# Kernel optimization log

Measured on AMD Instinct MI355X. Metric: run time of the kernel, lower is better.

## Reference

```python
import jax, jax.numpy as jnp
import numpy as np

EMBED = 256
HEADS = 8
LEVELS = 4
POINTS = 4
HD = EMBED // HEADS  # 32


def _bilinear_sample(v, grid):
    """torch.F.grid_sample(mode='bilinear', padding_mode='zeros', align_corners=False).
    v: (B, C, H, W); grid: (B, Q, P, 2) with xy coords in [-1, 1].
    Returns (B, C, Q, P).
    """
    B, C, H, W = v.shape
    x = (grid[..., 0] + 1.0) * (W * 0.5) - 0.5
    y = (grid[..., 1] + 1.0) * (H * 0.5) - 0.5
    x0f = jnp.floor(x)
    y0f = jnp.floor(y)
    wx = x - x0f
    wy = y - y0f
    x0 = x0f.astype(jnp.int32)
    y0 = y0f.astype(jnp.int32)
    vf = v.reshape(B, C, H * W)

    def corner(xi, yi, w):
        valid = (xi >= 0) & (xi < W) & (yi >= 0) & (yi < H)
        idx = jnp.clip(yi, 0, H - 1) * W + jnp.clip(xi, 0, W - 1)  # (B, Q, P)
        g = jax.vmap(lambda vb, ib: jnp.take(vb, ib, axis=1))(vf, idx.reshape(B, -1))
        g = g.reshape(B, C, idx.shape[1], idx.shape[2])  # (B, C, Q, P)
        return g * (w * valid.astype(v.dtype))[:, None]

    return (corner(x0, y0, (1 - wx) * (1 - wy))
            + corner(x0 + 1, y0, wx * (1 - wy))
            + corner(x0, y0 + 1, (1 - wx) * wy)
            + corner(x0 + 1, y0 + 1, wx * wy))


def setup_inputs() -> dict:
    key = jax.random.key(0)
    ks = jax.random.split(key, 16)
    N, Q, D = 2, 8192, EMBED
    inp = {
        'query': jax.random.normal(ks[0], (N, Q, D), jnp.float32),
        'feat0': jax.random.normal(ks[1], (N, D, 64, 64), jnp.float32),
        'feat1': jax.random.normal(ks[2], (N, D, 32, 32), jnp.float32),
        'feat2': jax.random.normal(ks[3], (N, D, 16, 16), jnp.float32),
        'feat3': jax.random.normal(ks[4], (N, D, 8, 8), jnp.float32),
        'reference_points': jax.random.uniform(ks[5], (N, Q, 2), jnp.float32),
        # params stored as (in, out); equivalent math to torch Linear's x @ W.T + b
        'W_off': jax.random.normal(ks[6], (D, HEADS * LEVELS * POINTS * 2), jnp.float32) * 0.01,
        'b_off': jax.random.normal(ks[7], (HEADS * LEVELS * POINTS * 2,), jnp.float32) * 0.01,
        'W_attn': jax.random.normal(ks[8], (D, HEADS * LEVELS * POINTS), jnp.float32) * 0.02,
        'b_attn': jax.random.normal(ks[9], (HEADS * LEVELS * POINTS,), jnp.float32) * 0.02,
        'W_val': jax.random.normal(ks[10], (D, D), jnp.float32) * (1.0 / np.sqrt(D)),
        'b_val': jnp.zeros((D,), jnp.float32),
        'W_out': jax.random.normal(ks[11], (D, D), jnp.float32) * (1.0 / np.sqrt(D)),
        'b_out': jnp.zeros((D,), jnp.float32),
    }
    return inp


def reference(query, feat0, feat1, feat2, feat3, reference_points,
              W_off, b_off, W_attn, b_attn, W_val, b_val, W_out, b_out):
    feats = [feat0, feat1, feat2, feat3]
    N, Q, D = query.shape
    # offset / attention-weight projections
    off = (query @ W_off + b_off).reshape(N, Q, HEADS, LEVELS, POINTS, 2)
    attn = (query @ W_attn + b_attn).reshape(N, Q, HEADS, LEVELS, POINTS)
    # reference points (N,Q,2) -> (N,Q,L,2)
    ref = jnp.broadcast_to(reference_points[:, :, None, :], (N, Q, LEVELS, 2))
    # value projection (1x1 conv) per level, split heads -> (N*H, hd, H_l, W_l)
    vals = [(jnp.einsum('bchw,cd->bdhw', f, W_val) + b_val[None, :, None, None])
            .reshape(N * HEADS, HD, f.shape[2], f.shape[3]) for f in feats]
    # flatten batch*heads
    off = off.transpose(0, 2, 1, 3, 4, 5).reshape(N * HEADS, Q, LEVELS, POINTS, 2)
    attn = attn.transpose(0, 2, 1, 3, 4).reshape(N * HEADS, Q, LEVELS, POINTS)
    refh = jnp.broadcast_to(ref[:, None], (N, HEADS, Q, LEVELS, 2)).reshape(N * HEADS, Q, LEVELS, 2)
    loc = refh[:, :, :, None, :] + off                 # (NH, Q, L, P, 2) in [0,1]
    grid = 2.0 * loc - 1.0                             # [-1, 1]
    # per-level bilinear sampling -> (NH, hd, Q, L, P)
    sampled = jnp.stack([_bilinear_sample(vals[l], grid[:, :, l]) for l in range(LEVELS)], axis=-2)
    # softmax over levels*points
    aw = jax.nn.softmax(attn.reshape(N * HEADS, Q, LEVELS * POINTS), axis=-1)
    aw = jnp.nan_to_num(aw).reshape(N * HEADS, Q, LEVELS, POINTS)
    out = jnp.einsum('bcqlp,bqlp->bcq', sampled, aw)   # (NH, hd, Q)
    out = out.reshape(N, HEADS, HD, Q).transpose(0, 3, 1, 2).reshape(N, Q, D)
    return out @ W_out + b_out
```

## Files before the change

kernel.cpp:

```cpp
#include <hip/hip_runtime.h>
#include <math.h>

#define NB 2
#define QN 8192
#define DIM 256
#define S_TOT 5440

typedef unsigned int uint32;
typedef _Float16 f16;
typedef __attribute__((ext_vector_type(8))) _Float16 h8;
typedef __attribute__((ext_vector_type(2))) _Float16 h2;
typedef __attribute__((ext_vector_type(4))) float f32x4;
typedef __attribute__((ext_vector_type(4))) uint32 u32x4;

__global__ __launch_bounds__(256) void prep_w_kernel(
    const float* __restrict__ W_off, const float* __restrict__ W_attn,
    const float* __restrict__ W_val, const float* __restrict__ W_out,
    f16* __restrict__ Wcat_t, f16* __restrict__ Wval_t, f16* __restrict__ Wout_t) {
  const int t = blockIdx.x;
  const float* src; f16* dst; int S, tb;
  if (t < 8)       { src = W_off;  dst = Wcat_t;             S = 256; tb = t; }
  else if (t < 12) { src = W_attn; dst = Wcat_t + 256 * 256; S = 128; tb = t - 8; }
  else if (t < 20) { src = W_val;  dst = Wval_t;             S = 256; tb = t - 12; }
  else             { src = W_out;  dst = Wout_t;             S = 256; tb = t - 20; }
  const int s0 = tb * 32, c0 = blockIdx.y * 32;

  __shared__ float tile[32][33];
  const int tx = threadIdx.x & 31, ty = threadIdx.x >> 5;
#pragma unroll
  for (int j = 0; j < 4; ++j) {
    const int c = c0 + ty + j * 8;
    tile[ty + j * 8][tx] = src[(size_t)c * S + s0 + tx];
  }
  __syncthreads();
#pragma unroll
  for (int j = 0; j < 4; ++j) {
    const int srow = s0 + ty + j * 8;
    dst[(size_t)srow * 256 + c0 + tx] = (f16)tile[tx][ty + j * 8];
  }
}

__global__ __launch_bounds__(256) void gemm_fused_kernel(
    const float* __restrict__ f0, const float* __restrict__ f1,
    const float* __restrict__ f2, const float* __restrict__ f3,
    const float* __restrict__ query,
    const f16* __restrict__ Wval_t, const f16* __restrict__ Wcat_t,
    const float* __restrict__ b_val, const float* __restrict__ b_off,
    const float* __restrict__ b_attn,
    f16* __restrict__ vals, f16* __restrict__ offb, f16* __restrict__ attnb) {
  __shared__ f16 As[64][256];
  __shared__ f16 Bs[64][256];
  const int t = blockIdx.x;
  const int tid = threadIdx.x;
  const bool isval = (t < 170);
  const size_t r0 = (size_t)(isval ? t : t - 170) * 64;
  const int NC = isval ? 4 : 6;
  const f16* Bt = isval ? Wval_t : Wcat_t;

  const int row = tid >> 5, slot = tid & 31;
  const int lane = tid & 63;

  if (isval) {
    const int b = (t >= 85) ? 1 : 0;
    const int tl = t - 85 * b;
    const float* fsrc; int HW, sl0;
    if (tl < 64)      { fsrc = f0; HW = 4096; sl0 = tl * 64; }
    else if (tl < 80) { fsrc = f1; HW = 1024; sl0 = (tl - 64) * 64; }
    else if (tl < 84) { fsrc = f2; HW = 256;  sl0 = (tl - 80) * 64; }
    else              { fsrc = f3; HW = 64;   sl0 = 0; }
    fsrc += (size_t)b * 256 * HW + sl0;
    const int cw = (tid >> 6) * 64 + (lane >> 4);
    const int s4 = (lane & 15) * 4;
#pragma unroll
    for (int pass = 0; pass < 16; ++pass) {
      const int c = cw + pass * 4;
      const float4 v = *(const float4*)(fsrc + (size_t)c * HW + s4);
      const int sl = c >> 3;
#pragma unroll
      for (int j = 0; j < 4; ++j) {
        const int r = s4 + j;
        const int ph = (sl & 24) | ((sl ^ r) & 7);
        As[r][ph * 8 + (c & 7)] = (f16)((const float*)&v)[j];
      }
    }
  } else {
#pragma unroll
    for (int i = 0; i < 8; ++i) {
      const int r = i * 8 + row;
      const int ph = (slot & 24) | ((slot ^ r) & 7);
      const float* ga = query + (r0 + r) * 256 + slot * 8;
      const float4 u0 = *(const float4*)ga;
      const float4 u1 = *(const float4*)(ga + 4);
      h8 hv = {(f16)u0.x, (f16)u0.y, (f16)u0.z, (f16)u0.w,
               (f16)u1.x, (f16)u1.y, (f16)u1.z, (f16)u1.w};
      *(h8*)&As[r][ph * 8] = hv;
    }
  }

  const int wid = tid >> 6;
  const int wr = (wid >> 1) * 32, wc = (wid & 1) * 32;
  const int l15 = lane & 15, l4 = lane >> 4;

  u32x4 bpre[8];
#pragma unroll
  for (int i = 0; i < 8; ++i) {
    bpre[i] = *(const u32x4*)(Bt + (size_t)(i * 8 + row) * 256 + slot * 8);
  }

  h8 areg[8][2];

  for (int c = 0; c < NC; ++c) {
    __syncthreads();
#pragma unroll
    for (int i = 0; i < 8; ++i) {
      const int r = i * 8 + row;
      const int ph = (slot & 24) | ((slot ^ r) & 7);
      *(u32x4*)&Bs[r][ph * 8] = bpre[i];
    }
    __syncthreads();

    if (c + 1 < NC) {
#pragma unroll
      for (int i = 0; i < 8; ++i) {
        bpre[i] = *(const u32x4*)(Bt + (size_t)((c + 1) * 64 + i * 8 + row) * 256 + slot * 8);
      }
    }

    f32x4 acc[2][2] = {};
#pragma unroll
    for (int ks = 0; ks < 8; ++ks) {
      const int slot2 = ks * 4 + l4;
      if (c == 0) {
#pragma unroll
        for (int m = 0; m < 2; ++m) {
          const int r = wr + m * 16 + l15;
          const int ph = (slot2 & 24) | ((slot2 ^ r) & 7);
          areg[ks][m] = *(const h8*)&As[r][ph * 8];
        }
      }
      h8 b[2];
#pragma unroll
      for (int n = 0; n < 2; ++n) {
        const int r = wc + n * 16 + l15;
        const int ph = (slot2 & 24) | ((slot2 ^ r) & 7);
        b[n] = *(const h8*)&Bs[r][ph * 8];
      }
#pragma unroll
      for (int m = 0; m < 2; ++m)
#pragma unroll
        for (int n = 0; n < 2; ++n)
          acc[m][n] = __builtin_amdgcn_mfma_f32_16x16x32_f16(areg[ks][m], b[n], acc[m][n], 0, 0, 0);
    }

#pragma unroll
    for (int m = 0; m < 2; ++m)
#pragma unroll
      for (int n = 0; n < 2; ++n)
#pragma unroll
        for (int r = 0; r < 4; ++r) {
          const size_t rw = r0 + wr + m * 16 + l4 * 4 + r;
          const int col = c * 64 + wc + n * 16 + l15;
          const float v = acc[m][n][r];
          if (isval) {
            vals[rw * 256 + col] = (f16)(v + b_val[col]);
          } else if (col < 256) {
            offb[rw * 256 + col] = (f16)(v + b_off[col]);
          } else {
            attnb[rw * 128 + (col - 256)] = (f16)(v + b_attn[col - 256]);
          }
        }
  }
}

__global__ __launch_bounds__(256) void gemm_out_kernel(
    const f16* __restrict__ A, const f16* __restrict__ Bt,
    const float* __restrict__ bias, float* __restrict__ out) {
  __shared__ f16 As[64][256];
  __shared__ f16 Bs[64][256];
  const int tid = threadIdx.x;
  const size_t r0 = (size_t)blockIdx.x * 64;

  const int row = tid >> 5, slot = tid & 31;
#pragma unroll
  for (int i = 0; i < 8; ++i) {
    const int r = i * 8 + row;
    const int ph = (slot & 24) | ((slot ^ r) & 7);
    *(u32x4*)&As[r][ph * 8] = *(const u32x4*)(A + (r0 + r) * 256 + slot * 8);
  }

  const int wid = tid >> 6, lane = tid & 63;
  const int wr = (wid >> 1) * 32, wc = (wid & 1) * 32;
  const int l15 = lane & 15, l4 = lane >> 4;

  u32x4 bpre[8];
#pragma unroll
  for (int i = 0; i < 8; ++i) {
    bpre[i] = *(const u32x4*)(Bt + (size_t)(i * 8 + row) * 256 + slot * 8);
  }

  h8 areg[8][2];

  for (int c = 0; c < 4; ++c) {
    __syncthreads();
#pragma unroll
    for (int i = 0; i < 8; ++i) {
      const int r = i * 8 + row;
      const int ph = (slot & 24) | ((slot ^ r) & 7);
      *(u32x4*)&Bs[r][ph * 8] = bpre[i];
    }
    __syncthreads();

    if (c + 1 < 4) {
#pragma unroll
      for (int i = 0; i < 8; ++i) {
        bpre[i] = *(const u32x4*)(Bt + (size_t)((c + 1) * 64 + i * 8 + row) * 256 + slot * 8);
      }
    }

    f32x4 acc[2][2] = {};
#pragma unroll
    for (int ks = 0; ks < 8; ++ks) {
      const int slot2 = ks * 4 + l4;
      if (c == 0) {
#pragma unroll
        for (int m = 0; m < 2; ++m) {
          const int r = wr + m * 16 + l15;
          const int ph = (slot2 & 24) | ((slot2 ^ r) & 7);
          areg[ks][m] = *(const h8*)&As[r][ph * 8];
        }
      }
      h8 b[2];
#pragma unroll
      for (int n = 0; n < 2; ++n) {
        const int r = wc + n * 16 + l15;
        const int ph = (slot2 & 24) | ((slot2 ^ r) & 7);
        b[n] = *(const h8*)&Bs[r][ph * 8];
      }
#pragma unroll
      for (int m = 0; m < 2; ++m)
#pragma unroll
        for (int n = 0; n < 2; ++n)
          acc[m][n] = __builtin_amdgcn_mfma_f32_16x16x32_f16(areg[ks][m], b[n], acc[m][n], 0, 0, 0);
    }

#pragma unroll
    for (int m = 0; m < 2; ++m)
#pragma unroll
      for (int n = 0; n < 2; ++n)
#pragma unroll
        for (int r = 0; r < 4; ++r) {
          const size_t rw = r0 + wr + m * 16 + l4 * 4 + r;
          const int col = c * 64 + wc + n * 16 + l15;
          out[rw * 256 + col] = acc[m][n][r] + bias[col];
        }
  }
}

__global__ __launch_bounds__(256) void sample_kernel(
    const f16* __restrict__ vals, const f16* __restrict__ offb,
    const f16* __restrict__ attnb, const float* __restrict__ refp,
    f16* __restrict__ samp) {
  const int tid = threadIdx.x;
  const int g = tid & 15;
  const int grp = tid >> 4;
  const int h = grp & 7;
  const int half = tid >> 7;
  const int bi = blockIdx.x;
  const int b = (bi >> 2) & 1;
  const int wb = (bi >> 3) * 4 + (bi & 3);
  const int bq = b * QN + wb * 2 + half;

  __shared__ float4 wts[16][17];
  __shared__ int4 idxs[16][17];

  const float rx = refp[(size_t)bq * 2 + 0];
  const float ry = refp[(size_t)bq * 2 + 1];

  float logit = (float)attnb[(size_t)bq * 128 + h * 16 + g];
  float m = logit;
#pragma unroll
  for (int mask = 1; mask < 16; mask <<= 1)
    m = fmaxf(m, __shfl_xor(m, mask, 16));
  const float e = __expf(logit - m);
  float ssum = e;
#pragma unroll
  for (int mask = 1; mask < 16; mask <<= 1)
    ssum += __shfl_xor(ssum, mask, 16);
  const float aw = e / ssum;

  const h2 ov = *(const h2*)(offb + (size_t)bq * 256 + h * 32 + g * 2);
  const int l = g >> 2;
  const int Wl = 64 >> l;
  const int loff = (l == 0) ? 0 : (l == 1) ? 4096 : (l == 2) ? 5120 : 5376;

  const float px = (rx + (float)ov[0]) * (float)Wl - 0.5f;
  const float py = (ry + (float)ov[1]) * (float)Wl - 0.5f;
  const float fx = floorf(px), fy = floorf(py);
  const float wx = px - fx, wy = py - fy;
  const int x0 = (int)fx, y0 = (int)fy;
  const int x1 = x0 + 1, y1 = y0 + 1;
  const float vx0 = (x0 >= 0 && x0 < Wl) ? 1.f : 0.f;
  const float vx1 = (x1 >= 0 && x1 < Wl) ? 1.f : 0.f;
  const float vy0 = (y0 >= 0 && y0 < Wl) ? 1.f : 0.f;
  const float vy1 = (y1 >= 0 && y1 < Wl) ? 1.f : 0.f;
  const int cx0 = min(max(x0, 0), Wl - 1), cx1 = min(max(x1, 0), Wl - 1);
  const int cy0 = min(max(y0, 0), Wl - 1), cy1 = min(max(y1, 0), Wl - 1);
  const int base = b * S_TOT + loff;
  idxs[grp][g] = make_int4((base + cy0 * Wl + cx0) * 512,
                           (base + cy0 * Wl + cx1) * 512,
                           (base + cy1 * Wl + cx0) * 512,
                           (base + cy1 * Wl + cx1) * 512);
  wts[grp][g] = make_float4(aw * (1.f - wx) * (1.f - wy) * vx0 * vy0,
                            aw * wx * (1.f - wy) * vx1 * vy0,
                            aw * (1.f - wx) * wy * vx0 * vy1,
                            aw * wx * wy * vx1 * vy1);
  __syncthreads();

  const int c4 = g & 3, pc = g >> 2;
  const char* vb = (const char*)vals + (h * 64 + c4 * 16);

  float wv[16];
  int ids[16];
#pragma unroll
  for (int pt = 0; pt < 16; ++pt) {
    wv[pt] = ((const float*)&wts[grp][pt])[pc];
    ids[pt] = ((const int*)&idxs[grp][pt])[pc];
  }
  h8 vv[16];
#pragma unroll
  for (int pt = 0; pt < 16; ++pt) vv[pt] = *(const h8*)(vb + ids[pt]);

  float a[8] = {};
#pragma unroll
  for (int pt = 0; pt < 16; ++pt) {
#pragma unroll
    for (int k = 0; k < 8; ++k) a[k] = fmaf((float)vv[pt][k], wv[pt], a[k]);
  }
#pragma unroll
  for (int k = 0; k < 8; ++k) {
    a[k] += __shfl_xor(a[k], 4);
    a[k] += __shfl_xor(a[k], 8);
  }
  if (pc == 0) {
    h8 r;
#pragma unroll
    for (int k = 0; k < 8; ++k) r[k] = (f16)a[k];
    *(h8*)(samp + (size_t)bq * 256 + h * 32 + c4 * 8) = r;
  }
}

extern "C" void kernel_launch(void* const* d_in, const int* in_sizes, int n_in,
                              void* d_out, int out_size, void* d_ws, size_t ws_size,
                              hipStream_t stream) {
  const float* query = (const float*)d_in[0];
  const float* feat[4] = {(const float*)d_in[1], (const float*)d_in[2],
                          (const float*)d_in[3], (const float*)d_in[4]};
  const float* refp  = (const float*)d_in[5];
  const float* W_off = (const float*)d_in[6];
  const float* b_off = (const float*)d_in[7];
  const float* W_attn = (const float*)d_in[8];
  const float* b_attn = (const float*)d_in[9];
  const float* W_val = (const float*)d_in[10];
  const float* b_val = (const float*)d_in[11];
  const float* W_out = (const float*)d_in[12];
  const float* b_out = (const float*)d_in[13];
  float* out = (float*)d_out;

  f16* ws = (f16*)d_ws;
  f16* vals   = ws;
  f16* offb   = vals + (size_t)NB * S_TOT * 256;
  f16* samp   = offb + (size_t)NB * QN * 256;
  f16* attnb  = samp + (size_t)NB * QN * 256;
  f16* Wcat_t = attnb + (size_t)NB * QN * 128;
  f16* Wval_t = Wcat_t + 384 * 256;
  f16* Wout_t = Wval_t + 256 * 256;

  prep_w_kernel<<<dim3(28, 8), 256, 0, stream>>>(
      W_off, W_attn, W_val, W_out, Wcat_t, Wval_t, Wout_t);

  gemm_fused_kernel<<<170 + 256, 256, 0, stream>>>(
      feat[0], feat[1], feat[2], feat[3], query, Wval_t, Wcat_t,
      b_val, b_off, b_attn, vals, offb, attnb);

  sample_kernel<<<(NB * QN) / 2, 256, 0, stream>>>(vals, offb, attnb, refp, samp);

  gemm_out_kernel<<<(NB * QN) / 64, 256, 0, stream>>>(samp, Wout_t, b_out, out);
}
```

Before: 69.78 us.

## Drop LDS staging of B in GEMMs, shrink tiles, and use fp16 packed accumulation in sampler

Both GEMM kernels now read the transposed weight fragments straight from global memory (L2-resident) instead of staging B through shared memory with barriers. The query and output GEMMs use 32-row tiles with direct register loads of A, which doubles the grid size. The sampler accumulates in packed fp16 (h2) instead of fp32, and its block-to-query mapping is simplified to a linear order. This removes LDS traffic and syncs but trades them for redundant global loads of weights, lower accumulation precision, and a different access order in the sampler.

```diff
diff --git a/kernel.cpp b/kernel.cpp
--- a/kernel.cpp
+++ b/kernel.cpp
@@ -12,6 +12,12 @@
 typedef __attribute__((ext_vector_type(2))) _Float16 h2;
 typedef __attribute__((ext_vector_type(4))) float f32x4;
 typedef __attribute__((ext_vector_type(4))) uint32 u32x4;
+
+__device__ __forceinline__ h2 shfl_h2(h2 v, int mask) {
+  union { h2 h; int i; } u; u.h = v;
+  u.i = __shfl_xor(u.i, mask);
+  return u.h;
+}
 
 __global__ __launch_bounds__(256) void prep_w_kernel(
     const float* __restrict__ W_off, const float* __restrict__ W_attn,
@@ -49,18 +55,12 @@
     const float* __restrict__ b_attn,
     f16* __restrict__ vals, f16* __restrict__ offb, f16* __restrict__ attnb) {
   __shared__ f16 As[64][256];
-  __shared__ f16 Bs[64][256];
   const int t = blockIdx.x;
   const int tid = threadIdx.x;
-  const bool isval = (t < 170);
-  const size_t r0 = (size_t)(isval ? t : t - 170) * 64;
-  const int NC = isval ? 4 : 6;
-  const f16* Bt = isval ? Wval_t : Wcat_t;
-
-  const int row = tid >> 5, slot = tid & 31;
-  const int lane = tid & 63;
-
-  if (isval) {
+  const int lane = tid & 63, wid = tid >> 6;
+  const int l15 = lane & 15, l4 = lane >> 4;
+
+  if (t < 170) {
     const int b = (t >= 85) ? 1 : 0;
     const int tl = t - 85 * b;
     const float* fsrc; int HW, sl0;
@@ -69,8 +69,8 @@
     else if (tl < 84) { fsrc = f2; HW = 256;  sl0 = (tl - 80) * 64; }
     else              { fsrc = f3; HW = 64;   sl0 = 0; }
     fsrc += (size_t)b * 256 * HW + sl0;
-    const int cw = (tid >> 6) * 64 + (lane >> 4);
-    const int s4 = (lane & 15) * 4;
+    const int cw = wid * 64 + l4;
+    const int s4 = l15 * 4;
 #pragma unroll
     for (int pass = 0; pass < 16; ++pass) {
       const int c = cw + pass * 4;
@@ -83,91 +83,97 @@
         As[r][ph * 8 + (c & 7)] = (f16)((const float*)&v)[j];
       }
     }
+    __syncthreads();
+
+    const size_t r0 = (size_t)t * 64;
+    const int wr = (wid >> 1) * 32, wc = (wid & 1) * 32;
+    h8 areg[8][2];
+    for (int c = 0; c < 4; ++c) {
+      f32x4 acc[2][2] = {};
+#pragma unroll
+      for (int ks = 0; ks < 8; ++ks) {
+        const int slot2 = ks * 4 + l4;
+        if (c == 0) {
+#pragma unroll
+          for (int m = 0; m < 2; ++m) {
+            const int r = wr + m * 16 + l15;
+            const int ph = (slot2 & 24) | ((slot2 ^ r) & 7);
+            areg[ks][m] = *(const h8*)&As[r][ph * 8];
+          }
+        }
+        h8 bfr[2];
+#pragma unroll
+        for (int n = 0; n < 2; ++n) {
+          const int col = c * 64 + wc + n * 16 + l15;
+          bfr[n] = *(const h8*)(Wval_t + (size_t)col * 256 + slot2 * 8);
+        }
+#pragma unroll
+        for (int m = 0; m < 2; ++m)
+#pragma unroll
+          for (int n = 0; n < 2; ++n)
+            acc[m][n] = __builtin_amdgcn_mfma_f32_16x16x32_f16(areg[ks][m], bfr[n], acc[m][n], 0, 0, 0);
+      }
+#pragma unroll
+      for (int m = 0; m < 2; ++m)
+#pragma unroll
+        for (int n = 0; n < 2; ++n)
+#pragma unroll
+          for (int r = 0; r < 4; ++r) {
+            const size_t rw = r0 + wr + m * 16 + l4 * 4 + r;
+            const int col = c * 64 + wc + n * 16 + l15;
+            vals[rw * 256 + col] = (f16)(acc[m][n][r] + b_val[col]);
+          }
+    }
   } else {
-#pragma unroll
-    for (int i = 0; i < 8; ++i) {
-      const int r = i * 8 + row;
-      const int ph = (slot & 24) | ((slot ^ r) & 7);
-      const float* ga = query + (r0 + r) * 256 + slot * 8;
-      const float4 u0 = *(const float4*)ga;
-      const float4 u1 = *(const float4*)(ga + 4);
-      h8 hv = {(f16)u0.x, (f16)u0.y, (f16)u0.z, (f16)u0.w,
-               (f16)u1.x, (f16)u1.y, (f16)u1.z, (f16)u1.w};
-      *(h8*)&As[r][ph * 8] = hv;
-    }
-  }
-
-  const int wid = tid >> 6;
-  const int wr = (wid >> 1) * 32, wc = (wid & 1) * 32;
-  const int l15 = lane & 15, l4 = lane >> 4;
-
-  u32x4 bpre[8];
-#pragma unroll
-  for (int i = 0; i < 8; ++i) {
-    bpre[i] = *(const u32x4*)(Bt + (size_t)(i * 8 + row) * 256 + slot * 8);
-  }
-
-  h8 areg[8][2];
-
-  for (int c = 0; c < NC; ++c) {
-    __syncthreads();
-#pragma unroll
-    for (int i = 0; i < 8; ++i) {
-      const int r = i * 8 + row;
-      const int ph = (slot & 24) | ((slot ^ r) & 7);
-      *(u32x4*)&Bs[r][ph * 8] = bpre[i];
-    }
-    __syncthreads();
-
-    if (c + 1 < NC) {
-#pragma unroll
-      for (int i = 0; i < 8; ++i) {
-        bpre[i] = *(const u32x4*)(Bt + (size_t)((c + 1) * 64 + i * 8 + row) * 256 + slot * 8);
-      }
-    }
-
-    f32x4 acc[2][2] = {};
+    const int t2 = t - 170;
+    const size_t r0 = (size_t)t2 * 32;
+    const int wc0 = wid * 96;
+
+    h8 areg[8][2];
+#pragma unroll
+    for (int ks = 0; ks < 8; ++ks) {
+      const int k0 = (ks * 4 + l4) * 8;
+#pragma unroll
+      for (int m = 0; m < 2; ++m) {
+        const float* ga = query + (r0 + m * 16 + l15) * 256 + k0;
+        const float4 u0 = *(const float4*)ga;
+        const float4 u1 = *(const float4*)(ga + 4);
+        h8 hv = {(f16)u0.x, (f16)u0.y, (f16)u0.z, (f16)u0.w,
+                 (f16)u1.x, (f16)u1.y, (f16)u1.z, (f16)u1.w};
+        areg[ks][m] = hv;
+      }
+    }
+
+    f32x4 acc[2][6] = {};
 #pragma unroll
     for (int ks = 0; ks < 8; ++ks) {
       const int slot2 = ks * 4 + l4;
-      if (c == 0) {
-#pragma unroll
-        for (int m = 0; m < 2; ++m) {
-          const int r = wr + m * 16 + l15;
-          const int ph = (slot2 & 24) | ((slot2 ^ r) & 7);
-          areg[ks][m] = *(const h8*)&As[r][ph * 8];
-        }
-      }
-      h8 b[2];
-#pragma unroll
-      for (int n = 0; n < 2; ++n) {
-        const int r = wc + n * 16 + l15;
-        const int ph = (slot2 & 24) | ((slot2 ^ r) & 7);
-        b[n] = *(const h8*)&Bs[r][ph * 8];
+      h8 bfr[6];
+#pragma unroll
+      for (int n = 0; n < 6; ++n) {
+        const int col = wc0 + n * 16 + l15;
+        bfr[n] = *(const h8*)(Wcat_t + (size_t)col * 256 + slot2 * 8);
       }
 #pragma unroll
       for (int m = 0; m < 2; ++m)
 #pragma unroll
-        for (int n = 0; n < 2; ++n)
-          acc[m][n] = __builtin_amdgcn_mfma_f32_16x16x32_f16(areg[ks][m], b[n], acc[m][n], 0, 0, 0);
+        for (int n = 0; n < 6; ++n)
+          acc[m][n] = __builtin_amdgcn_mfma_f32_16x16x32_f16(areg[ks][m], bfr[n], acc[m][n], 0, 0, 0);
     }
 
 #pragma unroll
     for (int m = 0; m < 2; ++m)
 #pragma unroll
-      for (int n = 0; n < 2; ++n)
+      for (int n = 0; n < 6; ++n)
 #pragma unroll
         for (int r = 0; r < 4; ++r) {
-          const size_t rw = r0 + wr + m * 16 + l4 * 4 + r;
-          const int col = c * 64 + wc + n * 16 + l15;
+          const size_t rw = r0 + m * 16 + l4 * 4 + r;
+          const int col = wc0 + n * 16 + l15;
           const float v = acc[m][n][r];
-          if (isval) {
-            vals[rw * 256 + col] = (f16)(v + b_val[col]);
-          } else if (col < 256) {
+          if (col < 256)
             offb[rw * 256 + col] = (f16)(v + b_off[col]);
-          } else {
+          else
             attnb[rw * 128 + (col - 256)] = (f16)(v + b_attn[col - 256]);
-          }
         }
   }
 }
@@ -175,85 +181,48 @@
 __global__ __launch_bounds__(256) void gemm_out_kernel(
     const f16* __restrict__ A, const f16* __restrict__ Bt,
     const float* __restrict__ bias, float* __restrict__ out) {
-  __shared__ f16 As[64][256];
-  __shared__ f16 Bs[64][256];
   const int tid = threadIdx.x;
-  const size_t r0 = (size_t)blockIdx.x * 64;
-
-  const int row = tid >> 5, slot = tid & 31;
-#pragma unroll
-  for (int i = 0; i < 8; ++i) {
-    const int r = i * 8 + row;
-    const int ph = (slot & 24) | ((slot ^ r) & 7);
-    *(u32x4*)&As[r][ph * 8] = *(const u32x4*)(A + (r0 + r) * 256 + slot * 8);
-  }
-
-  const int wid = tid >> 6, lane = tid & 63;
-  const int wr = (wid >> 1) * 32, wc = (wid & 1) * 32;
+  const int lane = tid & 63, wid = tid >> 6;
   const int l15 = lane & 15, l4 = lane >> 4;
-
-  u32x4 bpre[8];
-#pragma unroll
-  for (int i = 0; i < 8; ++i) {
-    bpre[i] = *(const u32x4*)(Bt + (size_t)(i * 8 + row) * 256 + slot * 8);
-  }
+  const size_t r0 = (size_t)blockIdx.x * 32;
+  const int wc0 = wid * 64;
 
   h8 areg[8][2];
-
-  for (int c = 0; c < 4; ++c) {
-    __syncthreads();
-#pragma unroll
-    for (int i = 0; i < 8; ++i) {
-      const int r = i * 8 + row;
-      const int ph = (slot & 24) | ((slot ^ r) & 7);
-      *(u32x4*)&Bs[r][ph * 8] = bpre[i];
-    }
-    __syncthreads();
-
-    if (c + 1 < 4) {
-#pragma unroll
-      for (int i = 0; i < 8; ++i) {
-        bpre[i] = *(const u32x4*)(Bt + (size_t)((c + 1) * 64 + i * 8 + row) * 256 + slot * 8);
-      }
-    }
-
-    f32x4 acc[2][2] = {};
-#pragma unroll
-    for (int ks = 0; ks < 8; ++ks) {
-      const int slot2 = ks * 4 + l4;
-      if (c == 0) {
-#pragma unroll
-        for (int m = 0; m < 2; ++m) {
-          const int r = wr + m * 16 + l15;
-          const int ph = (slot2 & 24) | ((slot2 ^ r) & 7);
-          areg[ks][m] = *(const h8*)&As[r][ph * 8];
-        }
-      }
-      h8 b[2];
-#pragma unroll
-      for (int n = 0; n < 2; ++n) {
-        const int r = wc + n * 16 + l15;
-        const int ph = (slot2 & 24) | ((slot2 ^ r) & 7);
-        b[n] = *(const h8*)&Bs[r][ph * 8];
-      }
-#pragma unroll
-      for (int m = 0; m < 2; ++m)
-#pragma unroll
-        for (int n = 0; n < 2; ++n)
-          acc[m][n] = __builtin_amdgcn_mfma_f32_16x16x32_f16(areg[ks][m], b[n], acc[m][n], 0, 0, 0);
-    }
-
+#pragma unroll
+  for (int ks = 0; ks < 8; ++ks) {
+    const int k0 = (ks * 4 + l4) * 8;
 #pragma unroll
     for (int m = 0; m < 2; ++m)
-#pragma unroll
-      for (int n = 0; n < 2; ++n)
-#pragma unroll
-        for (int r = 0; r < 4; ++r) {
-          const size_t rw = r0 + wr + m * 16 + l4 * 4 + r;
-          const int col = c * 64 + wc + n * 16 + l15;
-          out[rw * 256 + col] = acc[m][n][r] + bias[col];
-        }
-  }
+      areg[ks][m] = *(const h8*)(A + (r0 + m * 16 + l15) * 256 + k0);
+  }
+
+  f32x4 acc[2][4] = {};
+#pragma unroll
+  for (int ks = 0; ks < 8; ++ks) {
+    const int slot2 = ks * 4 + l4;
+    h8 bfr[4];
+#pragma unroll
+    for (int n = 0; n < 4; ++n) {
+      const int col = wc0 + n * 16 + l15;
+      bfr[n] = *(const h8*)(Bt + (size_t)col * 256 + slot2 * 8);
+    }
+#pragma unroll
+    for (int m = 0; m < 2; ++m)
+#pragma unroll
+      for (int n = 0; n < 4; ++n)
+        acc[m][n] = __builtin_amdgcn_mfma_f32_16x16x32_f16(areg[ks][m], bfr[n], acc[m][n], 0, 0, 0);
+  }
+
+#pragma unroll
+  for (int m = 0; m < 2; ++m)
+#pragma unroll
+    for (int n = 0; n < 4; ++n)
+#pragma unroll
+      for (int r = 0; r < 4; ++r) {
+        const size_t rw = r0 + m * 16 + l4 * 4 + r;
+        const int col = wc0 + n * 16 + l15;
+        out[rw * 256 + col] = acc[m][n][r] + bias[col];
+      }
 }
 
 __global__ __launch_bounds__(256) void sample_kernel(
@@ -265,10 +234,8 @@
   const int grp = tid >> 4;
   const int h = grp & 7;
   const int half = tid >> 7;
-  const int bi = blockIdx.x;
-  const int b = (bi >> 2) & 1;
-  const int wb = (bi >> 3) * 4 + (bi & 3);
-  const int bq = b * QN + wb * 2 + half;
+  const int bq = blockIdx.x * 2 + half;
+  const int b = bq >> 13;
 
   __shared__ float4 wts[16][17];
   __shared__ int4 idxs[16][17];
@@ -330,21 +297,25 @@
 #pragma unroll
   for (int pt = 0; pt < 16; ++pt) vv[pt] = *(const h8*)(vb + ids[pt]);
 
-  float a[8] = {};
+  h2 a2[4] = {};
 #pragma unroll
   for (int pt = 0; pt < 16; ++pt) {
-#pragma unroll
-    for (int k = 0; k < 8; ++k) a[k] = fmaf((float)vv[pt][k], wv[pt], a[k]);
-  }
-#pragma unroll
-  for (int k = 0; k < 8; ++k) {
-    a[k] += __shfl_xor(a[k], 4);
-    a[k] += __shfl_xor(a[k], 8);
+    const f16 wh = (f16)wv[pt];
+    const h2 w2 = {wh, wh};
+    const h2* vp = (const h2*)&vv[pt];
+    a2[0] += vp[0] * w2;
+    a2[1] += vp[1] * w2;
+    a2[2] += vp[2] * w2;
+    a2[3] += vp[3] * w2;
+  }
+#pragma unroll
+  for (int j = 0; j < 4; ++j) {
+    a2[j] += shfl_h2(a2[j], 4);
+    a2[j] += shfl_h2(a2[j], 8);
   }
   if (pc == 0) {
-    h8 r;
-#pragma unroll
-    for (int k = 0; k < 8; ++k) r[k] = (f16)a[k];
+    h8 r = {a2[0][0], a2[0][1], a2[1][0], a2[1][1],
+            a2[2][0], a2[2][1], a2[3][0], a2[3][1]};
     *(h8*)(samp + (size_t)bq * 256 + h * 32 + c4 * 8) = r;
   }
 }
@@ -378,11 +349,11 @@
   prep_w_kernel<<<dim3(28, 8), 256, 0, stream>>>(
       W_off, W_attn, W_val, W_out, Wcat_t, Wval_t, Wout_t);
 
-  gemm_fused_kernel<<<170 + 256, 256, 0, stream>>>(
+  gemm_fused_kernel<<<170 + 512, 256, 0, stream>>>(
       feat[0], feat[1], feat[2], feat[3], query, Wval_t, Wcat_t,
       b_val, b_off, b_attn, vals, offb, attnb);
 
   sample_kernel<<<(NB * QN) / 2, 256, 0, stream>>>(vals, offb, attnb, refp, samp);
 
-  gemm_out_kernel<<<(NB * QN) / 64, 256, 0, stream>>>(samp, Wout_t, b_out, out);
-}
+  gemm_out_kernel<<<(NB * QN) / 32, 256, 0, stream>>>(samp, Wout_t, b_out, out);
+}
```

New measurement: 85.83 us. +23.0%, slower.
